# Kernel tuning notes

Hardware: AMD Instinct MI355X
Metric: run time of the kernel (lower is better)

Reference implementation:

```python
import jax, jax.numpy as jnp
import numpy as np

D_IN = 1024
D_OUT = 1024
NUM_HEADS = 16
HEAD_DIM = D_OUT // NUM_HEADS
CONTEXT_LEN = 2048


def setup_inputs() -> dict:
    key = jax.random.key(0)
    ks = jax.random.split(key, 7)
    scale = 0.02
    x = jax.random.normal(ks[0], (2, 2048, D_IN), dtype=jnp.float32)
    Wq = jax.random.normal(ks[1], (D_IN, D_OUT), dtype=jnp.float32) * scale
    bq = jnp.zeros((D_OUT,), dtype=jnp.float32)
    Wk = jax.random.normal(ks[2], (D_IN, D_OUT), dtype=jnp.float32) * scale
    bk = jnp.zeros((D_OUT,), dtype=jnp.float32)
    Wv = jax.random.normal(ks[3], (D_IN, D_OUT), dtype=jnp.float32) * scale
    bv = jnp.zeros((D_OUT,), dtype=jnp.float32)
    return {"x": x, "Wq": Wq, "bq": bq, "Wk": Wk, "bk": bk, "Wv": Wv, "bv": bv}


def reference(x, Wq, bq, Wk, bk, Wv, bv):
    B, S, _ = x.shape
    # QKV projections with bias
    q = x @ Wq + bq  # [B,S,D_OUT]
    k = x @ Wk + bk
    v = x @ Wv + bv
    # split heads -> [B,H,S,Dh]
    def heads(t):
        return t.reshape(B, S, NUM_HEADS, HEAD_DIM).transpose(0, 2, 1, 3)
    q, k, v = heads(q), heads(k), heads(v)
    # raw scores, then additive causal mask (-1e9 on strictly upper triangle),
    # then scale by 1/sqrt(head_dim) AFTER adding mask (matches original code)
    scores = jnp.einsum("bhqd,bhkd->bhqk", q, k)
    causal = jnp.tril(jnp.ones((S, S), dtype=bool))
    add_mask = jnp.where(causal, 0.0, -1e9).astype(scores.dtype)
    scores = scores + add_mask
    weights = jax.nn.softmax(scores / jnp.sqrt(jnp.asarray(HEAD_DIM, scores.dtype)), axis=-1)
    ctx = jnp.einsum("bhqk,bhkd->bhqd", weights, v)  # [B,H,S,Dh]
    return ctx.transpose(0, 2, 1, 3).reshape(B, S, D_OUT)
```

## Files before the change

kernel.cpp:

```cpp
#include <hip/hip_runtime.h>
#include <hip/hip_bf16.h>
#include <stdint.h>

#define D_IN 1024
#define NH 16
#define DH 64
#define SEQ 2048
#define BATCH 2

typedef unsigned short u16;
typedef __attribute__((ext_vector_type(8))) short short8;
typedef __attribute__((ext_vector_type(4))) float f32x4;

#define CSCALE 0.1803368801f

__device__ __forceinline__ u16 f2bf(float f) {
    union { float f; uint32_t u; } v; v.f = f;
    uint32_t r = v.u + 0x7FFF + ((v.u >> 16) & 1);
    return (u16)(r >> 16);
}

__device__ __forceinline__ float bf2f(u16 u) {
    union { uint32_t u; float f; } v; v.u = (uint32_t)u << 16;
    return v.f;
}

__device__ __forceinline__ uint32_t pktrunc(float a, float b) {
    union { float f; uint32_t u; } x, y;
    x.f = a; y.f = b;
    return __builtin_amdgcn_perm(y.u, x.u, 0x07060302u);
}

__device__ __forceinline__ void async16(const u16* g, u16* l) {
    __builtin_amdgcn_global_load_lds(
        (const __attribute__((address_space(1))) void*)g,
        (__attribute__((address_space(3))) void*)l, 16, 0, 0);
}

__global__ __launch_bounds__(256) void prep_kernel(
    const float* __restrict__ x, const float* __restrict__ Wq,
    const float* __restrict__ Wk, const float* __restrict__ Wv,
    u16* __restrict__ xb, u16* __restrict__ WT)
{
    __shared__ float tile[64][65];
    if (blockIdx.x < 4096) {
        int i = (blockIdx.x * 256 + threadIdx.x) * 4;
        float4 v = *(const float4*)(x + i);
        union { u16 u[4]; uint2 d; } o;
        o.u[0] = f2bf(v.x); o.u[1] = f2bf(v.y); o.u[2] = f2bf(v.z); o.u[3] = f2bf(v.w);
        *(uint2*)(xb + i) = o.d;
        return;
    }
    int idx = blockIdx.x - 4096;
    int mat = idx >> 8, rem = idx & 255;
    int k0 = (rem & 15) * 64, n0 = (rem >> 4) * 64;
    const float* W = (mat == 0) ? Wq : (mat == 1 ? Wk : Wv);
    int c = threadIdx.x & 63, rb = threadIdx.x >> 6;
    #pragma unroll
    for (int p = 0; p < 16; ++p) {
        int r = p * 4 + rb;
        tile[r][c] = W[(size_t)(k0 + r) * 1024 + n0 + c];
    }
    __syncthreads();
    #pragma unroll
    for (int p = 0; p < 16; ++p) {
        int r = p * 4 + rb;
        WT[((size_t)mat * 1024 + n0 + r) * 1024 + k0 + c] = f2bf(tile[c][r]);
    }
}

__global__ __launch_bounds__(512, 2) void qkv_gemm_kernel(
    const u16* __restrict__ xb, const u16* __restrict__ WT,
    const float* __restrict__ bq, const float* __restrict__ bk,
    const float* __restrict__ bv,
    u16* __restrict__ Qb, u16* __restrict__ Kb, u16* __restrict__ Vt)
{
    __shared__ u16 smem[65536];
    u16* As = smem;
    u16* Bs = smem + 32768;

    const int tid  = threadIdx.x;
    const int wave = tid >> 6, lane = tid & 63;
    const int quad = lane >> 4, l15 = lane & 15;
    const int wm = wave >> 2, wn = wave & 3;
    const int fsig = l15 & 7;

    const int lin = blockIdx.x;
    const int logical = (lin & 7) * 24 + (lin >> 3);
    const int by = logical / 12;
    const int bx = logical % 12;
    const int m0 = by * 256;
    const int n0 = bx * 256;

    const int ch  = tid & 7;
    const int rwT = tid >> 3;

    f32x4 acc[8][4];
    #pragma unroll
    for (int i = 0; i < 8; ++i)
        #pragma unroll
        for (int j = 0; j < 4; ++j)
            acc[i][j] = (f32x4){0.f, 0.f, 0.f, 0.f};

    auto stageA = [&](int buf, int kst) {
        #pragma unroll
        for (int r = 0; r < 4; ++r) {
            int row = r * 64 + rwT;
            int g = ch ^ (row & 7);
            async16(xb + (size_t)(m0 + row) * 1024 + kst + g * 8,
                    As + buf * 16384 + row * 64 + ch * 8);
        }
    };
    auto stageBh = [&](int buf, int kst, int half) {
        #pragma unroll
        for (int r = 0; r < 2; ++r) {
            int row = half * 128 + r * 64 + rwT;
            int g = ch ^ (row & 7);
            async16(WT + (size_t)(n0 + row) * 1024 + kst + g * 8,
                    Bs + buf * 16384 + row * 64 + ch * 8);
        }
    };

    stageA(0, 0);  stageBh(0, 0, 0);  stageBh(0, 0, 1);
    stageA(1, 64); stageBh(1, 64, 0); stageBh(1, 64, 1);
    asm volatile("s_waitcnt vmcnt(8)" ::: "memory");
    __builtin_amdgcn_sched_barrier(0);
    __builtin_amdgcn_s_barrier();

    for (int t = 0; t < 16; ++t) {
        const int cur = t & 1;
        const u16* Ab = As + cur * 16384;
        const u16* Bb = Bs + cur * 16384;
        const bool st = (t + 2 < 16);
        const int k2 = (t + 2) * 64;

        short8 bfr[4][2];
        #pragma unroll
        for (int j = 0; j < 4; ++j)
            #pragma unroll
            for (int kk = 0; kk < 2; ++kk)
                bfr[j][kk] = *(const short8*)(Bb + (wn * 64 + j * 16 + l15) * 64 +
                                              (((kk << 2) + quad) ^ fsig) * 8);

        #pragma unroll
        for (int p = 0; p < 4; ++p) {
            short8 af[2][2];
            #pragma unroll
            for (int i2 = 0; i2 < 2; ++i2)
                #pragma unroll
                for (int kk = 0; kk < 2; ++kk)
                    af[i2][kk] = *(const short8*)(Ab + (wm * 128 + (p * 2 + i2) * 16 + l15) * 64 +
                                                  (((kk << 2) + quad) ^ fsig) * 8);
            if (p == 1 && st) stageBh(cur, k2, 0);
            if (p == 2 && st) stageBh(cur, k2, 1);
            __builtin_amdgcn_s_barrier();
            if (p == 3 && st) stageA(cur, k2);
            __builtin_amdgcn_s_setprio(1);
            #pragma unroll
            for (int kk = 0; kk < 2; ++kk)
                #pragma unroll
                for (int i2 = 0; i2 < 2; ++i2)
                    #pragma unroll
                    for (int j = 0; j < 4; ++j)
                        acc[p * 2 + i2][j] = __builtin_amdgcn_mfma_f32_16x16x32_bf16(
                            af[i2][kk], bfr[j][kk], acc[p * 2 + i2][j], 0, 0, 0);
            __builtin_amdgcn_s_setprio(0);
            if (p == 3) {
                if (st)            { asm volatile("s_waitcnt vmcnt(8)" ::: "memory"); }
                else if (t == 14)  { asm volatile("s_waitcnt vmcnt(0)" ::: "memory"); }
                __builtin_amdgcn_sched_barrier(0);
            }
            __builtin_amdgcn_s_barrier();
        }
    }
    __syncthreads();

    const int mat = n0 >> 10;
    const int ncb = (n0 & 1023) + wn * 64;
    const int hh = ncb >> 6;
    const int bb = m0 >> 11, sb = m0 & 2047;

    if (mat < 2) {
        const float* bias = (mat == 0) ? bq : bk;
        u16* dst = (mat == 0) ? Qb : Kb;
        const float sc = (mat == 0) ? CSCALE : 1.0f;
        #pragma unroll
        for (int i = 0; i < 8; ++i) {
            int ss = sb + wm * 128 + i * 16 + quad * 4;
            #pragma unroll
            for (int j = 0; j < 4; ++j) {
                int dh = j * 16 + l15;
                float bval = bias[ncb + dh];
                size_t base = (((size_t)bb * NH + hh) * SEQ + ss) * DH + dh;
                #pragma unroll
                for (int r = 0; r < 4; ++r)
                    dst[base + (size_t)r * DH] = f2bf((acc[i][j][r] + bval) * sc);
            }
        }
    } else {
        u16* vt = smem + wave * (64 * 72);
        u16* vdst = Vt + ((size_t)(bb * NH + hh) * DH) * SEQ;
        #pragma unroll
        for (int h2 = 0; h2 < 2; ++h2) {
            #pragma unroll
            for (int i = 0; i < 4; ++i)
                #pragma unroll
                for (int j = 0; j < 4; ++j) {
                    float bval = bv[ncb + j * 16 + l15];
                    union { u16 u[4]; uint2 d; } o;
                    #pragma unroll
                    for (int r = 0; r < 4; ++r)
                        o.u[r] = f2bf(acc[h2 * 4 + i][j][r] + bval);
                    *(uint2*)(vt + (j * 16 + l15) * 72 + i * 16 + quad * 4) = o.d;
                }
            const int s0w = sb + wm * 128 + h2 * 64;
            #pragma unroll
            for (int it = 0; it < 8; ++it) {
                int dh = it * 8 + (lane >> 3);
                short8 v = *(const short8*)(vt + dh * 72 + (lane & 7) * 8);
                *(short8*)(vdst + (size_t)dh * SEQ + s0w + (lane & 7) * 8) = v;
            }
        }
    }
}

__device__ __forceinline__ void stage64(const u16* g0, size_t gstride, u16* lds,
                                        int wave, int lane)
{
    #pragma unroll
    for (int rnd = 0; rnd < 2; ++rnd) {
        int row = rnd * 32 + wave * 8 + (lane >> 3);
        int sig = ((row >> 3) & 1) * 4 + (row & 3);
        int c = (lane & 7) ^ sig;
        async16(g0 + (size_t)row * gstride + c * 8, lds + row * 64 + (lane & 7) * 8);
    }
}

__global__ __launch_bounds__(256) void flash_mfma_kernel(
    const u16* __restrict__ Qb, const u16* __restrict__ Kb,
    const u16* __restrict__ Vt, float* __restrict__ out,
    u16* __restrict__ Opart, float* __restrict__ Lpart)
{
    static const int JQT[24] = {7,15,15,14,14, 6,13,13,12,12, 5,11,11,10,10,
                                4, 9, 9, 8, 8, 3, 2, 1, 0};
    static const int JHF[24] = {-1,0,1,0,1, -1,0,1,0,1, -1,0,1,0,1,
                                -1,0,1,0,1, -1,-1,-1,-1};

    __shared__ u16 Ks[2][64 * 64];
    __shared__ u16 Vs[2][64 * 64];

    const int tid  = threadIdx.x;
    const int wave = tid >> 6, lane = tid & 63;
    const int quad = lane >> 4, l15 = lane & 15;
    const int bhx = blockIdx.x;
    const int b = bhx >> 4, h = bhx & 15;
    const int job = blockIdx.y;
    const int qt = JQT[job], hf = JHF[job];
    const int t0 = (hf == 1) ? qt + 1 : 0;
    const int t1 = (hf == 0) ? qt + 1 : 2 * qt + 2;
    const int q0 = qt * 128;
    const int wq0 = wave * 32;
    const size_t bh = (size_t)bhx;
    const u16* Qp = Qb + bh * SEQ * DH;
    const u16* Kp = Kb + bh * SEQ * DH;
    const u16* Vp = Vt + bh * DH * SEQ;

    short8 qf[2][2];
    #pragma unroll
    for (int qa = 0; qa < 2; ++qa) {
        const u16* qrp = Qp + (size_t)(q0 + wq0 + qa * 16 + l15) * DH;
        qf[qa][0] = *(const short8*)(qrp + quad * 8);
        qf[qa][1] = *(const short8*)(qrp + 32 + quad * 8);
    }

    const short8 ones = (short8){0x3F80, 0x3F80, 0x3F80, 0x3F80,
                                 0x3F80, 0x3F80, 0x3F80, 0x3F80};

    f32x4 O[2][4], L[2];
    #pragma unroll
    for (int pa = 0; pa < 2; ++pa) {
        #pragma unroll
        for (int f = 0; f < 4; ++f) O[pa][f] = (f32x4){0.f, 0.f, 0.f, 0.f};
        L[pa] = (f32x4){0.f, 0.f, 0.f, 0.f};
    }

    const int wqmax = q0 + wq0 + 31;
    const int krbase = (l15 >> 2) * 8 + (l15 & 3);
    const int ksig   = ((l15 >> 2) & 1) * 4 + (l15 & 3);
    const int vsig   = ((l15 >> 3) & 1) * 4 + (l15 & 3);

    stage64(Kp + (size_t)t0 * 64 * DH, DH, Ks[t0 & 1], wave, lane);
    stage64(Vp + t0 * 64, SEQ, Vs[t0 & 1], wave, lane);
    __syncthreads();

    for (int t = t0; t < t1; ++t) {
        const int cur = t & 1;
        if (t + 1 < t1) {
            int k1 = (t + 1) * 64;
            stage64(Kp + (size_t)k1 * DH, DH, Ks[cur ^ 1], wave, lane);
            stage64(Vp + k1, SEQ, Vs[cur ^ 1], wave, lane);
        }
        const int k0 = t * 64;
        if (k0 <= wqmax) {
            f32x4 sf[4][2];
            #pragma unroll
            for (int fj = 0; fj < 4; ++fj) {
                int krow = (fj >> 1) * 32 + krbase + (fj & 1) * 4;
                const u16* kp = &Ks[cur][krow * 64];
                short8 k0f = *(const short8*)(kp + (quad ^ ksig) * 8);
                short8 k1f = *(const short8*)(kp + ((4 + quad) ^ ksig) * 8);
                #pragma unroll
                for (int qa = 0; qa < 2; ++qa) {
                    f32x4 s = (f32x4){0.f, 0.f, 0.f, 0.f};
                    s = __builtin_amdgcn_mfma_f32_16x16x32_bf16(k0f, qf[qa][0], s, 0, 0, 0);
                    s = __builtin_amdgcn_mfma_f32_16x16x32_bf16(k1f, qf[qa][1], s, 0, 0, 0);
                    sf[fj][qa] = s;
                }
            }
            const bool diag = (k0 + 63 > q0 + wq0);
            short8 pA[2][2];
            #pragma unroll
            for (int qa = 0; qa < 2; ++qa) {
                #pragma unroll
                for (int fj = 0; fj < 4; ++fj)
                    #pragma unroll
                    for (int r = 0; r < 4; ++r) {
                        float p = __builtin_amdgcn_exp2f(sf[fj][qa][r]);
                        if (diag) {
                            int key = k0 + (fj >> 1) * 32 + quad * 8 + (fj & 1) * 4 + r;
                            int qg  = q0 + wq0 + qa * 16 + l15;
                            p = (key <= qg) ? p : 0.f;
                        }
                        sf[fj][qa][r] = p;
                    }
                union { uint32_t d[4]; short8 v; } a0, a1;
                a0.d[0] = pktrunc(sf[0][qa][0], sf[0][qa][1]);
                a0.d[1] = pktrunc(sf[0][qa][2], sf[0][qa][3]);
                a0.d[2] = pktrunc(sf[1][qa][0], sf[1][qa][1]);
                a0.d[3] = pktrunc(sf[1][qa][2], sf[1][qa][3]);
                a1.d[0] = pktrunc(sf[2][qa][0], sf[2][qa][1]);
                a1.d[1] = pktrunc(sf[2][qa][2], sf[2][qa][3]);
                a1.d[2] = pktrunc(sf[3][qa][0], sf[3][qa][1]);
                a1.d[3] = pktrunc(sf[3][qa][2], sf[3][qa][3]);
                pA[qa][0] = a0.v;
                pA[qa][1] = a1.v;
                L[qa] = __builtin_amdgcn_mfma_f32_16x16x32_bf16(pA[qa][0], ones, L[qa], 0, 0, 0);
                L[qa] = __builtin_amdgcn_mfma_f32_16x16x32_bf16(pA[qa][1], ones, L[qa], 0, 0, 0);
            }
            #pragma unroll
            for (int fo = 0; fo < 4; ++fo) {
                const u16* vrow = &Vs[cur][(fo * 16 + l15) * 64];
                short8 vb0 = *(const short8*)(vrow + (quad ^ vsig) * 8);
                short8 vb1 = *(const short8*)(vrow + ((4 + quad) ^ vsig) * 8);
                #pragma unroll
                for (int pa = 0; pa < 2; ++pa) {
                    O[pa][fo] = __builtin_amdgcn_mfma_f32_16x16x32_bf16(pA[pa][0], vb0, O[pa][fo], 0, 0, 0);
                    O[pa][fo] = __builtin_amdgcn_mfma_f32_16x16x32_bf16(pA[pa][1], vb1, O[pa][fo], 0, 0, 0);
                }
            }
        }
        __syncthreads();
    }

    if (hf < 0) {
        #pragma unroll
        for (int pa = 0; pa < 2; ++pa)
            #pragma unroll
            for (int fo = 0; fo < 4; ++fo)
                #pragma unroll
                for (int r = 0; r < 4; ++r) {
                    int s = q0 + wq0 + pa * 16 + quad * 4 + r;
                    out[((size_t)b * SEQ + s) * 1024 + h * DH + fo * 16 + l15] =
                        O[pa][fo][r] / L[pa][r];
                }
    } else {
        const int pi = (qt - 8) * 2 + hf;
        u16* op = Opart + (((size_t)pi * 32 + bhx) * 128) * 64;
        float* lp = Lpart + ((size_t)pi * 32 + bhx) * 128;
        #pragma unroll
        for (int pa = 0; pa < 2; ++pa) {
            #pragma unroll
            for (int fo = 0; fo < 4; ++fo)
                #pragma unroll
                for (int r = 0; r < 4; ++r) {
                    int ql = wq0 + pa * 16 + quad * 4 + r;
                    op[(size_t)ql * 64 + fo * 16 + l15] = f2bf(O[pa][fo][r]);
                }
            if (l15 == 0) {
                #pragma unroll
                for (int r = 0; r < 4; ++r)
                    lp[wq0 + pa * 16 + quad * 4 + r] = L[pa][r];
            }
        }
    }
}

__global__ __launch_bounds__(256) void combine_kernel(
    const u16* __restrict__ Opart, const float* __restrict__ Lpart,
    float* __restrict__ out)
{
    int blk = blockIdx.x;
    int qt = 8 + (blk >> 5);
    int bh = blk & 31;
    int b = bh >> 4, h = bh & 15;
    int pi0 = (qt - 8) * 2, pi1 = pi0 + 1;
    int tid = threadIdx.x;
    int q = tid >> 1, seg = (tid & 1) * 32;
    const u16* o0 = Opart + (((size_t)pi0 * 32 + bh) * 128 + q) * 64 + seg;
    const u16* o1 = Opart + (((size_t)pi1 * 32 + bh) * 128 + q) * 64 + seg;
    float inv = 1.0f / (Lpart[((size_t)pi0 * 32 + bh) * 128 + q] +
                        Lpart[((size_t)pi1 * 32 + bh) * 128 + q]);
    float* op = out + ((size_t)b * SEQ + qt * 128 + q) * 1024 + h * DH + seg;
    #pragma unroll
    for (int d = 0; d < 32; d += 4) {
        union { uint2 d2; u16 u[4]; } a, c;
        a.d2 = *(const uint2*)(o0 + d);
        c.d2 = *(const uint2*)(o1 + d);
        float4 v;
        v.x = (bf2f(a.u[0]) + bf2f(c.u[0])) * inv;
        v.y = (bf2f(a.u[1]) + bf2f(c.u[1])) * inv;
        v.z = (bf2f(a.u[2]) + bf2f(c.u[2])) * inv;
        v.w = (bf2f(a.u[3]) + bf2f(c.u[3])) * inv;
        *(float4*)(op + d) = v;
    }
}

extern "C" void kernel_launch(void* const* d_in, const int* in_sizes, int n_in,
                              void* d_out, int out_size, void* d_ws, size_t ws_size,
                              hipStream_t stream) {
    const float* x  = (const float*)d_in[0];
    const float* Wq = (const float*)d_in[1];
    const float* bq = (const float*)d_in[2];
    const float* Wk = (const float*)d_in[3];
    const float* bk = (const float*)d_in[4];
    const float* Wv = (const float*)d_in[5];
    const float* bv = (const float*)d_in[6];
    float* out = (float*)d_out;

    const size_t NX = (size_t)BATCH * SEQ * D_IN;
    const size_t NW = (size_t)3 * D_IN * 1024;
    const size_t NP = (size_t)BATCH * NH * SEQ * DH;
    u16* xb = (u16*)d_ws;
    u16* WT = xb + NX;
    u16* Qb = WT + NW;
    u16* Kb = Qb + NP;
    u16* Vt = Kb + NP;
    u16* Opart = xb;
    float* Lpart = (float*)(xb + NX);

    prep_kernel<<<4096 + 768, 256, 0, stream>>>(x, Wq, Wk, Wv, xb, WT);
    qkv_gemm_kernel<<<dim3(192), 512, 0, stream>>>(xb, WT, bq, bk, bv, Qb, Kb, Vt);
    flash_mfma_kernel<<<dim3(32, 24), 256, 0, stream>>>(Qb, Kb, Vt, out, Opart, Lpart);
    combine_kernel<<<256, 256, 0, stream>>>(Opart, Lpart, out);
}
```

Measured before the change: 156.2 us.

## Software-pipeline QK^T of next tile with softmax/PV of previous tile

Restructures the attention loop so the QK^T MFMAs for tile t are issued before the exp/mask/PV work for tile t-1, using two score register sets and a triple-buffered V tile in LDS. The loop barrier is replaced by an explicit vmcnt wait, sched_barrier and s_barrier. The aim is to overlap the matrix work with the exponent and packing ALU work across tiles. In exchange it holds a second set of scores in registers, which may raise register pressure and lower occupancy, and it uses more LDS for the extra V buffer.

```diff
diff --git a/kernel.cpp b/kernel.cpp
--- a/kernel.cpp
+++ b/kernel.cpp
@@ -247,7 +247,7 @@
                                 -1,0,1,0,1, -1,-1,-1,-1};
 
     __shared__ u16 Ks[2][64 * 64];
-    __shared__ u16 Vs[2][64 * 64];
+    __shared__ u16 Vs[3][64 * 64];
 
     const int tid  = threadIdx.x;
     const int wave = tid >> 6, lane = tid & 63;
@@ -289,78 +289,105 @@
     const int ksig   = ((l15 >> 2) & 1) * 4 + (l15 & 3);
     const int vsig   = ((l15 >> 3) & 1) * 4 + (l15 & 3);
 
+    auto qkTile = [&](f32x4 (&sf)[4][2], int t) {
+        const u16* kb = Ks[t & 1];
+        #pragma unroll
+        for (int fj = 0; fj < 4; ++fj) {
+            int krow = (fj >> 1) * 32 + krbase + (fj & 1) * 4;
+            const u16* kp = kb + krow * 64;
+            short8 k0f = *(const short8*)(kp + (quad ^ ksig) * 8);
+            short8 k1f = *(const short8*)(kp + ((4 + quad) ^ ksig) * 8);
+            #pragma unroll
+            for (int qa = 0; qa < 2; ++qa) {
+                f32x4 s = (f32x4){0.f, 0.f, 0.f, 0.f};
+                s = __builtin_amdgcn_mfma_f32_16x16x32_bf16(k0f, qf[qa][0], s, 0, 0, 0);
+                s = __builtin_amdgcn_mfma_f32_16x16x32_bf16(k1f, qf[qa][1], s, 0, 0, 0);
+                sf[fj][qa] = s;
+            }
+        }
+    };
+
+    auto finishTile = [&](f32x4 (&sf)[4][2], int tp) {
+        const int kb0 = tp * 64;
+        const bool diag = (kb0 + 63 > q0 + wq0);
+        const u16* vbase = Vs[tp % 3];
+        short8 pA[2][2];
+        #pragma unroll
+        for (int qa = 0; qa < 2; ++qa) {
+            #pragma unroll
+            for (int fj = 0; fj < 4; ++fj)
+                #pragma unroll
+                for (int r = 0; r < 4; ++r) {
+                    float p = __builtin_amdgcn_exp2f(sf[fj][qa][r]);
+                    if (diag) {
+                        int key = kb0 + (fj >> 1) * 32 + quad * 8 + (fj & 1) * 4 + r;
+                        int qg  = q0 + wq0 + qa * 16 + l15;
+                        p = (key <= qg) ? p : 0.f;
+                    }
+                    sf[fj][qa][r] = p;
+                }
+            union { uint32_t d[4]; short8 v; } a0, a1;
+            a0.d[0] = pktrunc(sf[0][qa][0], sf[0][qa][1]);
+            a0.d[1] = pktrunc(sf[0][qa][2], sf[0][qa][3]);
+            a0.d[2] = pktrunc(sf[1][qa][0], sf[1][qa][1]);
+            a0.d[3] = pktrunc(sf[1][qa][2], sf[1][qa][3]);
+            a1.d[0] = pktrunc(sf[2][qa][0], sf[2][qa][1]);
+            a1.d[1] = pktrunc(sf[2][qa][2], sf[2][qa][3]);
+            a1.d[2] = pktrunc(sf[3][qa][0], sf[3][qa][1]);
+            a1.d[3] = pktrunc(sf[3][qa][2], sf[3][qa][3]);
+            pA[qa][0] = a0.v;
+            pA[qa][1] = a1.v;
+            L[qa] = __builtin_amdgcn_mfma_f32_16x16x32_bf16(pA[qa][0], ones, L[qa], 0, 0, 0);
+            L[qa] = __builtin_amdgcn_mfma_f32_16x16x32_bf16(pA[qa][1], ones, L[qa], 0, 0, 0);
+        }
+        #pragma unroll
+        for (int fo = 0; fo < 4; ++fo) {
+            const u16* vrow = vbase + (fo * 16 + l15) * 64;
+            short8 vb0 = *(const short8*)(vrow + (quad ^ vsig) * 8);
+            short8 vb1 = *(const short8*)(vrow + ((4 + quad) ^ vsig) * 8);
+            #pragma unroll
+            for (int pa = 0; pa < 2; ++pa) {
+                O[pa][fo] = __builtin_amdgcn_mfma_f32_16x16x32_bf16(pA[pa][0], vb0, O[pa][fo], 0, 0, 0);
+                O[pa][fo] = __builtin_amdgcn_mfma_f32_16x16x32_bf16(pA[pa][1], vb1, O[pa][fo], 0, 0, 0);
+            }
+        }
+    };
+
     stage64(Kp + (size_t)t0 * 64 * DH, DH, Ks[t0 & 1], wave, lane);
-    stage64(Vp + t0 * 64, SEQ, Vs[t0 & 1], wave, lane);
-    __syncthreads();
+    stage64(Vp + t0 * 64, SEQ, Vs[t0 % 3], wave, lane);
+    asm volatile("s_waitcnt vmcnt(0)" ::: "memory");
+    __builtin_amdgcn_sched_barrier(0);
+    __builtin_amdgcn_s_barrier();
+
+    f32x4 sA[4][2], sB[4][2];
+    int tpA = -1, tpB = -1;
 
     for (int t = t0; t < t1; ++t) {
-        const int cur = t & 1;
-        if (t + 1 < t1) {
+        const bool st = (t + 1 < t1);
+        if (st) {
             int k1 = (t + 1) * 64;
-            stage64(Kp + (size_t)k1 * DH, DH, Ks[cur ^ 1], wave, lane);
-            stage64(Vp + k1, SEQ, Vs[cur ^ 1], wave, lane);
+            stage64(Kp + (size_t)k1 * DH, DH, Ks[(t + 1) & 1], wave, lane);
+            stage64(Vp + k1, SEQ, Vs[(t + 1) % 3], wave, lane);
         }
         const int k0 = t * 64;
-        if (k0 <= wqmax) {
-            f32x4 sf[4][2];
-            #pragma unroll
-            for (int fj = 0; fj < 4; ++fj) {
-                int krow = (fj >> 1) * 32 + krbase + (fj & 1) * 4;
-                const u16* kp = &Ks[cur][krow * 64];
-                short8 k0f = *(const short8*)(kp + (quad ^ ksig) * 8);
-                short8 k1f = *(const short8*)(kp + ((4 + quad) ^ ksig) * 8);
-                #pragma unroll
-                for (int qa = 0; qa < 2; ++qa) {
-                    f32x4 s = (f32x4){0.f, 0.f, 0.f, 0.f};
-                    s = __builtin_amdgcn_mfma_f32_16x16x32_bf16(k0f, qf[qa][0], s, 0, 0, 0);
-                    s = __builtin_amdgcn_mfma_f32_16x16x32_bf16(k1f, qf[qa][1], s, 0, 0, 0);
-                    sf[fj][qa] = s;
-                }
-            }
-            const bool diag = (k0 + 63 > q0 + wq0);
-            short8 pA[2][2];
-            #pragma unroll
-            for (int qa = 0; qa < 2; ++qa) {
-                #pragma unroll
-                for (int fj = 0; fj < 4; ++fj)
-                    #pragma unroll
-                    for (int r = 0; r < 4; ++r) {
-                        float p = __builtin_amdgcn_exp2f(sf[fj][qa][r]);
-                        if (diag) {
-                            int key = k0 + (fj >> 1) * 32 + quad * 8 + (fj & 1) * 4 + r;
-                            int qg  = q0 + wq0 + qa * 16 + l15;
-                            p = (key <= qg) ? p : 0.f;
-                        }
-                        sf[fj][qa][r] = p;
-                    }
-                union { uint32_t d[4]; short8 v; } a0, a1;
-                a0.d[0] = pktrunc(sf[0][qa][0], sf[0][qa][1]);
-                a0.d[1] = pktrunc(sf[0][qa][2], sf[0][qa][3]);
-                a0.d[2] = pktrunc(sf[1][qa][0], sf[1][qa][1]);
-                a0.d[3] = pktrunc(sf[1][qa][2], sf[1][qa][3]);
-                a1.d[0] = pktrunc(sf[2][qa][0], sf[2][qa][1]);
-                a1.d[1] = pktrunc(sf[2][qa][2], sf[2][qa][3]);
-                a1.d[2] = pktrunc(sf[3][qa][0], sf[3][qa][1]);
-                a1.d[3] = pktrunc(sf[3][qa][2], sf[3][qa][3]);
-                pA[qa][0] = a0.v;
-                pA[qa][1] = a1.v;
-                L[qa] = __builtin_amdgcn_mfma_f32_16x16x32_bf16(pA[qa][0], ones, L[qa], 0, 0, 0);
-                L[qa] = __builtin_amdgcn_mfma_f32_16x16x32_bf16(pA[qa][1], ones, L[qa], 0, 0, 0);
-            }
-            #pragma unroll
-            for (int fo = 0; fo < 4; ++fo) {
-                const u16* vrow = &Vs[cur][(fo * 16 + l15) * 64];
-                short8 vb0 = *(const short8*)(vrow + (quad ^ vsig) * 8);
-                short8 vb1 = *(const short8*)(vrow + ((4 + quad) ^ vsig) * 8);
-                #pragma unroll
-                for (int pa = 0; pa < 2; ++pa) {
-                    O[pa][fo] = __builtin_amdgcn_mfma_f32_16x16x32_bf16(pA[pa][0], vb0, O[pa][fo], 0, 0, 0);
-                    O[pa][fo] = __builtin_amdgcn_mfma_f32_16x16x32_bf16(pA[pa][1], vb1, O[pa][fo], 0, 0, 0);
-                }
-            }
-        }
-        __syncthreads();
-    }
+        const bool cmp = (k0 <= wqmax);
+        if (((t - t0) & 1) == 0) {
+            if (cmp) qkTile(sA, t);
+            if (tpB >= 0) { finishTile(sB, tpB); tpB = -1; }
+            if (cmp) tpA = t;
+        } else {
+            if (cmp) qkTile(sB, t);
+            if (tpA >= 0) { finishTile(sA, tpA); tpA = -1; }
+            if (cmp) tpB = t;
+        }
+        if (st) {
+            asm volatile("s_waitcnt vmcnt(0)" ::: "memory");
+            __builtin_amdgcn_sched_barrier(0);
+            __builtin_amdgcn_s_barrier();
+        }
+    }
+    if (tpA >= 0) finishTile(sA, tpA);
+    if (tpB >= 0) finishTile(sB, tpB);
 
     if (hf < 0) {
         #pragma unroll
```

Result: slower. 189.8 us (+21.5%).
